# Kernel tuning notes

Hardware: AMD Instinct MI355X
Metric: run time of the kernel (lower is better)

Reference implementation:

```python
import jax, jax.numpy as jnp
import numpy as np

DIM = 1024          # moe_cfg.dim
INTER = 1024        # moe_cfg.moe_inter_dim
E = 8               # moe_cfg.n_routed_experts
TOPK = 2            # moe_cfg.n_activated_experts
ROUTE_SCALE = 1.0
SHARED_INTER = 2048 # n_shared_experts * moe_inter_dim
B, S = 4, 2048


def setup_inputs() -> dict:
    key = jax.random.key(0)
    ks = jax.random.split(key, 10)
    def w(k, shape, scale=0.02):
        return jax.random.normal(k, shape, jnp.float32) * scale
    return {
        "x": jax.random.normal(ks[0], (B, S, DIM), jnp.float32),
        # Gate (nn.Linear(dim, n_routed_experts, bias=True))
        "gate_w": w(ks[1], (E, DIM)),
        "gate_b": jnp.zeros((E,), jnp.float32),
        # Routed experts, stacked on leading E axis (torch Linear convention: [out, in])
        "w1": w(ks[2], (E, INTER, DIM)), "b1": jnp.zeros((E, INTER), jnp.float32),
        "w3": w(ks[3], (E, INTER, DIM)), "b3": jnp.zeros((E, INTER), jnp.float32),
        "w2": w(ks[4], (E, DIM, INTER)), "b2": jnp.zeros((E, DIM), jnp.float32),
        # Shared expert MLP(dim, n_shared_experts * moe_inter_dim)
        "ws1": w(ks[5], (SHARED_INTER, DIM)), "bs1": jnp.zeros((SHARED_INTER,), jnp.float32),
        "ws3": w(ks[6], (SHARED_INTER, DIM)), "bs3": jnp.zeros((SHARED_INTER,), jnp.float32),
        "ws2": w(ks[7], (DIM, SHARED_INTER)), "bs2": jnp.zeros((DIM,), jnp.float32),
    }


def _moe_forward(x, gate_w, gate_b, w1, b1, w3, b3, w2, b2,
                 ws1, bs1, ws3, bs3, ws2, bs2):
    Bq, Sq, D = x.shape
    xt = x.reshape(-1, D)  # [T, D], T = B*S
    # ---- Gate: softmax scores in fp32, top-k routing (eval mode: no usage buffers) ----
    logits = (xt @ gate_w.T + gate_b).astype(jnp.float32)  # [T, E]
    scores = jax.nn.softmax(logits, axis=-1)
    top_w, top_i = jax.lax.top_k(scores, TOPK)             # values == gathered scores
    weights = (top_w * ROUTE_SCALE).astype(x.dtype)        # [T, topk]
    # Dense combine weights [T, E]: zero for unrouted experts (math identical to dispatch)
    gate_dense = jnp.sum(jax.nn.one_hot(top_i, E, dtype=x.dtype) * weights[..., None], axis=1)
    # ---- Routed experts: SwiGLU FFN per expert (dropout p=0 -> identity) ----
    def expert(w1e, b1e, w3e, b3e, w2e, b2e):
        h = jax.nn.silu(xt @ w1e.T + b1e) * (xt @ w3e.T + b3e)  # [T, INTER]
        return h @ w2e.T + b2e                                   # [T, D]
    outs = jax.vmap(expert)(w1, b1, w3, b3, w2, b2)  # [E, T, D]
    y = jnp.einsum('etd,te->td', outs, gate_dense)   # weighted combine
    # ---- Shared expert MLP (SwiGLU) ----
    z = (jax.nn.silu(xt @ ws1.T + bs1) * (xt @ ws3.T + bs3)) @ ws2.T + bs2
    return (y + z).reshape(Bq, Sq, D)


def reference(x, gate_w, gate_b, w1, b1, w3, b3, w2, b2,
              ws1, bs1, ws3, bs3, ws2, bs2):
    return _moe_forward(x, gate_w, gate_b, w1, b1, w3, b3, w2, b2,
                        ws1, bs1, ws3, bs3, ws2, bs2)
```

## Files before the change

### kernel.cpp

```cpp
#include <hip/hip_runtime.h>
#include <stdint.h>
#include <stddef.h>

#define T_TOK  8192
#define DIMK   1024
#define INTERK 1024
#define NEXP   8
#define SINT   2048
#define CAP    18432
#define RT256  72

typedef float  f32x4  __attribute__((ext_vector_type(4)));
typedef short  bf16x8 __attribute__((ext_vector_type(8)));

typedef __attribute__((address_space(1))) const unsigned int gas_u32;
typedef __attribute__((address_space(3))) unsigned int las_u32;

__device__ __forceinline__ void gload16(const void* g, void* l) {
  __builtin_amdgcn_global_load_lds((gas_u32*)g, (las_u32*)l, 16, 0, 0);
}

__device__ __forceinline__ unsigned short f2b(float f) {
  unsigned int u = __float_as_uint(f);
  u = (u + 0x7FFFu + ((u >> 16) & 1u)) >> 16;
  return (unsigned short)u;
}
__device__ __forceinline__ float b2f(unsigned short h) {
  return __uint_as_float(((unsigned int)h) << 16);
}

__device__ __forceinline__ void barrier_nodrain() {
  asm volatile("" ::: "memory");
  __builtin_amdgcn_s_barrier();
  asm volatile("" ::: "memory");
}

__global__ __launch_bounds__(256) void cvt_kernel(const float4* __restrict__ in,
                                                  unsigned short* __restrict__ out, int n4) {
  int i = blockIdx.x * 256 + threadIdx.x;
  if (i >= n4) return;
  float4 v = in[i];
  ushort4 o;
  o.x = f2b(v.x); o.y = f2b(v.y); o.z = f2b(v.z); o.w = f2b(v.w);
  *reinterpret_cast<ushort4*>(&out[(size_t)i * 4]) = o;
}

template <int ROWS_PER_E, int K4>
__global__ __launch_bounds__(256) void cvt_w13_kernel(
    const float4* __restrict__ w1, const float4* __restrict__ w3,
    unsigned short* __restrict__ out, int n ) {
  int idx = blockIdx.x * 256 + threadIdx.x;
  int is3 = idx >= n;
  int i = is3 ? idx - n : idx;
  if (i >= n) return;
  int r  = i / K4;
  int kc = i - r * K4;
  int e  = r / ROWS_PER_E;
  int rr = r - e * ROWS_PER_E;
  int g  = rr >> 4;
  size_t dst_r = (size_t)e * (2 * ROWS_PER_E) + g * 32 + (is3 ? 16 : 0) + (rr & 15);
  float4 v = (is3 ? w3 : w1)[i];
  ushort4 o;
  o.x = f2b(v.x); o.y = f2b(v.y); o.z = f2b(v.z); o.w = f2b(v.w);
  *reinterpret_cast<ushort4*>(&out[(dst_r * K4 + kc) * 4]) = o;
}

__global__ __launch_bounds__(256) void gate_kernel(
    const float* __restrict__ x, const float* __restrict__ gw, const float* __restrict__ gb,
    int* __restrict__ top_i, float* __restrict__ top_w) {
  int t    = blockIdx.x * 4 + (threadIdx.x >> 6);
  int lane = threadIdx.x & 63;
  const float* xr = x + (size_t)t * DIMK;
  float acc[NEXP];
#pragma unroll
  for (int e = 0; e < NEXP; ++e) acc[e] = 0.f;
  for (int i = lane; i < DIMK; i += 64) {
    float xv = xr[i];
#pragma unroll
    for (int e = 0; e < NEXP; ++e) acc[e] += xv * gw[e * DIMK + i];
  }
#pragma unroll
  for (int e = 0; e < NEXP; ++e) {
    float v = acc[e];
#pragma unroll
    for (int off = 32; off > 0; off >>= 1) v += __shfl_down(v, off, 64);
    acc[e] = v;
  }
  if (lane == 0) {
    float lg[NEXP];
#pragma unroll
    for (int e = 0; e < NEXP; ++e) lg[e] = acc[e] + gb[e];
    int i0 = 0;
#pragma unroll
    for (int e = 1; e < NEXP; ++e) if (lg[e] > lg[i0]) i0 = e;
    int i1 = (i0 == 0) ? 1 : 0;
#pragma unroll
    for (int e = 0; e < NEXP; ++e) if (e != i0 && lg[e] > lg[i1]) i1 = e;
    float mx = lg[i0], s = 0.f;
#pragma unroll
    for (int e = 0; e < NEXP; ++e) s += expf(lg[e] - mx);
    top_i[t * 2]     = i0;
    top_i[t * 2 + 1] = i1;
    top_w[t * 2]     = expf(lg[i0] - mx) / s;
    top_w[t * 2 + 1] = expf(lg[i1] - mx) / s;
  }
}

__global__ __launch_bounds__(512) void route_build_kernel(
    const int* __restrict__ top_i, int* __restrict__ order, int* __restrict__ pos,
    int* __restrict__ poff_g) {
  __shared__ int cnt[NEXP][512];
  __shared__ int base[NEXP][512];
  __shared__ int totals[NEXP];
  __shared__ int poff_s[NEXP + 1];
  int tid = threadIdx.x;
  int lane = tid & 63, w = tid >> 6;
  const int t0 = tid * 16;

  int c[NEXP];
#pragma unroll
  for (int e = 0; e < NEXP; ++e) c[e] = 0;
  for (int j = 0; j < 16; ++j) {
    int e0 = top_i[(t0 + j) * 2];
    int e1 = top_i[(t0 + j) * 2 + 1];
#pragma unroll
    for (int e = 0; e < NEXP; ++e) c[e] += (e0 == e) + (e1 == e);
  }
#pragma unroll
  for (int e = 0; e < NEXP; ++e) cnt[e][tid] = c[e];
  __syncthreads();

  {
    int running = 0;
    for (int ch = 0; ch < 8; ++ch) {
      int v = cnt[w][ch * 64 + lane];
      int incl = v;
#pragma unroll
      for (int off = 1; off < 64; off <<= 1) {
        int u = __shfl_up(incl, off, 64);
        if (lane >= off) incl += u;
      }
      base[w][ch * 64 + lane] = running + incl - v;
      running += __shfl(incl, 63, 64);
    }
    if (lane == 0) totals[w] = running;
  }
  __syncthreads();

  if (tid == 0) {
    int off = 0;
#pragma unroll
    for (int e = 0; e < NEXP; ++e) {
      poff_s[e] = off;
      off += (totals[e] + 255) & ~255;
    }
    poff_s[NEXP] = off;
#pragma unroll
    for (int e = 0; e <= NEXP; ++e) poff_g[e] = poff_s[e];
  }
  __syncthreads();

  int cur[NEXP];
#pragma unroll
  for (int e = 0; e < NEXP; ++e) cur[e] = poff_s[e] + base[e][tid];
  for (int j = 0; j < 16; ++j) {
    int t = t0 + j;
#pragma unroll
    for (int k = 0; k < 2; ++k) {
      int ei = top_i[t * 2 + k];
      int p = 0;
#pragma unroll
      for (int e = 0; e < NEXP; ++e)
        if (ei == e) { p = cur[e]; cur[e] = p + 1; }
      order[p]       = t;
      pos[t * 2 + k] = p;
    }
  }

#pragma unroll
  for (int e = 0; e < NEXP; ++e) {
    int s = poff_s[e] + totals[e], en = poff_s[e + 1];
    for (int i = s + tid; i < en; i += 512) order[i] = 0;
  }
}

#define A_ELE  16384
#define B_ELE  8192
template <bool EXPERTS, bool GATHER, int EPI>
__global__ __launch_bounds__(512) void gemm256_kernel(
    const unsigned short* __restrict__ A, int lda,
    const int* __restrict__ order, const int* __restrict__ poff,
    const unsigned short* __restrict__ B,
    const float* __restrict__ bias1, const float* __restrict__ bias3,
    size_t wstride, int bstride, int K,
    void* __restrict__ outp, int ldo) {
  __shared__ unsigned short lds[2 * A_ELE + 2 * B_ELE];

  int rowbase = blockIdx.x * 256;
  int expert  = 0;
  if (EXPERTS) {
    if (rowbase >= poff[NEXP]) return;
    while (expert < NEXP - 1 && rowbase >= poff[expert + 1]) ++expert;
  }
  const unsigned short* Be = B + (size_t)expert * wstride;

  int tid = threadIdx.x;
  int lane = tid & 63, wid = tid >> 6;
  int wr = wid >> 1, wc = wid & 1;
  int ncolbase = blockIdx.y * 128;

  size_t aoff[4], boff[2];
#pragma unroll
  for (int l = 0; l < 4; ++l) {
    int g = l * 512 + tid;
    int r = g >> 3;
    int sub = (g & 7) ^ (r & 7);
    int gr = GATHER ? order[rowbase + r] : (rowbase + r);
    aoff[l] = (size_t)gr * lda + (size_t)(sub * 8);
  }
#pragma unroll
  for (int l = 0; l < 2; ++l) {
    int g = l * 512 + tid;
    int r = g >> 3;
    int sub = (g & 7) ^ (r & 7);
    boff[l] = (size_t)(ncolbase + r) * K + (size_t)(sub * 8);
  }

  f32x4 acc[4][4];
#pragma unroll
  for (int m = 0; m < 4; ++m)
#pragma unroll
    for (int n = 0; n < 4; ++n) acc[m][n] = f32x4{0.f, 0.f, 0.f, 0.f};

  const int NT = K >> 6;

#pragma unroll
  for (int l = 0; l < 4; ++l)
    gload16(A + aoff[l], &lds[(size_t)(l * 512 + tid) * 8]);
#pragma unroll
  for (int l = 0; l < 2; ++l)
    gload16(Be + boff[l], &lds[2 * A_ELE + (size_t)(l * 512 + tid) * 8]);

  for (int t = 0; t < NT; ++t) {
    int cur = t & 1;
    if (t + 1 < NT) {
      int kb = (t + 1) << 6;
      int nxt = cur ^ 1;
#pragma unroll
      for (int l = 0; l < 4; ++l)
        gload16(A + aoff[l] + kb, &lds[(size_t)nxt * A_ELE + (size_t)(l * 512 + tid) * 8]);
#pragma unroll
      for (int l = 0; l < 2; ++l)
        gload16(Be + boff[l] + kb, &lds[2 * A_ELE + (size_t)nxt * B_ELE + (size_t)(l * 512 + tid) * 8]);
      asm volatile("s_waitcnt vmcnt(6)" ::: "memory");
    } else {
      asm volatile("s_waitcnt vmcnt(0)" ::: "memory");
    }
    barrier_nodrain();

    const unsigned short* Ab = &lds[(size_t)cur * A_ELE];
    const unsigned short* Bb = &lds[2 * A_ELE + (size_t)cur * B_ELE];
    __builtin_amdgcn_s_setprio(1);
#pragma unroll
    for (int kk = 0; kk < 2; ++kk) {
      bf16x8 a[4], b[4];
#pragma unroll
      for (int m = 0; m < 4; ++m) {
        int ra = wr * 64 + m * 16 + (lane & 15);
        int sa = (kk * 4 + (lane >> 4)) ^ (ra & 7);
        a[m] = *(const bf16x8*)&Ab[ra * 64 + sa * 8];
      }
#pragma unroll
      for (int n = 0; n < 4; ++n) {
        int rb = wc * 64 + n * 16 + (lane & 15);
        int sb = (kk * 4 + (lane >> 4)) ^ (rb & 7);
        b[n] = *(const bf16x8*)&Bb[rb * 64 + sb * 8];
      }
#pragma unroll
      for (int m = 0; m < 4; ++m)
#pragma unroll
        for (int n = 0; n < 4; ++n)
          acc[m][n] = __builtin_amdgcn_mfma_f32_16x16x32_bf16(a[m], b[n], acc[m][n], 0, 0, 0);
    }
    __builtin_amdgcn_s_setprio(0);
    asm volatile("s_waitcnt lgkmcnt(0)" ::: "memory");
    barrier_nodrain();
  }

  if (EPI == 0) {
#pragma unroll
    for (int m = 0; m < 4; ++m)
#pragma unroll
      for (int np = 0; np < 2; ++np) {
        int realcol = (ncolbase >> 1) + wc * 32 + np * 16 + (lane & 15);
        float bb1 = bias1[bstride * expert + realcol];
        float bb3 = bias3[bstride * expert + realcol];
#pragma unroll
        for (int j = 0; j < 4; ++j) {
          int row  = rowbase + wr * 64 + m * 16 + (lane >> 4) * 4 + j;
          float a1 = acc[m][2 * np][j] + bb1;
          float a3 = acc[m][2 * np + 1][j] + bb3;
          float hv = (a1 / (1.f + __expf(-a1))) * a3;
          ((unsigned short*)outp)[(size_t)row * ldo + realcol] = f2b(hv);
        }
      }
  } else {
#pragma unroll
    for (int m = 0; m < 4; ++m)
#pragma unroll
      for (int n = 0; n < 4; ++n) {
        int col  = ncolbase + wc * 64 + n * 16 + (lane & 15);
        float bb = bias1[bstride * expert + col];
#pragma unroll
        for (int j = 0; j < 4; ++j) {
          int row = rowbase + wr * 64 + m * 16 + (lane >> 4) * 4 + j;
          float v = acc[m][n][j] + bb;
          if (EPI == 2)
            ((float*)outp)[(size_t)row * ldo + col] = v;
          else
            ((unsigned short*)outp)[(size_t)row * ldo + col] = f2b(v);
        }
      }
  }
}

__global__ __launch_bounds__(256) void combine_kernel(
    float* __restrict__ out, const unsigned short* __restrict__ y,
    const int* __restrict__ pos, const float* __restrict__ tw) {
  size_t idx = (size_t)blockIdx.x * 256 + threadIdx.x;
  if (idx >= (size_t)T_TOK * DIMK) return;
  int t = (int)(idx >> 10);
  int d = (int)(idx & 1023);
  int p0 = pos[t * 2], p1 = pos[t * 2 + 1];
  float w0 = tw[t * 2], w1 = tw[t * 2 + 1];
  out[idx] += w0 * b2f(y[(size_t)p0 * DIMK + d]) + w1 * b2f(y[(size_t)p1 * DIMK + d]);
}

extern "C" void kernel_launch(void* const* d_in, const int* in_sizes, int n_in,
                              void* d_out, int out_size, void* d_ws, size_t ws_size,
                              hipStream_t stream) {
  const float* x   = (const float*)d_in[0];
  const float* gw  = (const float*)d_in[1];
  const float* gb  = (const float*)d_in[2];
  const float* w1  = (const float*)d_in[3];
  const float* b1  = (const float*)d_in[4];
  const float* w3  = (const float*)d_in[5];
  const float* b3  = (const float*)d_in[6];
  const float* w2  = (const float*)d_in[7];
  const float* b2  = (const float*)d_in[8];
  const float* ws1 = (const float*)d_in[9];
  const float* bs1 = (const float*)d_in[10];
  const float* ws3 = (const float*)d_in[11];
  const float* bs3 = (const float*)d_in[12];
  const float* ws2 = (const float*)d_in[13];
  const float* bs2 = (const float*)d_in[14];
  float* out = (float*)d_out;
  (void)in_sizes; (void)n_in; (void)out_size; (void)ws_size;

  char* p = (char*)d_ws;
  auto alloc = [&](size_t bytes) -> void* {
    void* r = (void*)p;
    p += (bytes + 255) & ~(size_t)255;
    return r;
  };
  unsigned short* xb    = (unsigned short*)alloc((size_t)T_TOK * DIMK * 2);
  unsigned short* w13r  = (unsigned short*)alloc((size_t)NEXP * 2 * INTERK * DIMK * 2);
  unsigned short* w2b   = (unsigned short*)alloc((size_t)NEXP * DIMK * INTERK * 2);
  unsigned short* w13s  = (unsigned short*)alloc((size_t)2 * SINT * DIMK * 2);
  unsigned short* ws2b  = (unsigned short*)alloc((size_t)DIMK * SINT * 2);
  unsigned short* h     = (unsigned short*)alloc((size_t)CAP * INTERK * 2);
  unsigned short* yb    = (unsigned short*)alloc((size_t)CAP * DIMK * 2);
  unsigned short* hs    = (unsigned short*)alloc((size_t)T_TOK * SINT * 2);
  int*   top_i  = (int*)alloc((size_t)T_TOK * 2 * 4);
  float* top_w  = (float*)alloc((size_t)T_TOK * 2 * 4);
  int*   pos    = (int*)alloc((size_t)T_TOK * 2 * 4);
  int*   order  = (int*)alloc((size_t)CAP * 4);
  int*   poff   = (int*)alloc(64);

  auto cvt = [&](const float* src, unsigned short* dst, size_t n) {
    int n4 = (int)(n / 4);
    cvt_kernel<<<(n4 + 255) / 256, 256, 0, stream>>>((const float4*)src, dst, n4);
  };
  cvt(x,   xb,   (size_t)T_TOK * DIMK);
  cvt(w2,  w2b,  (size_t)NEXP * DIMK * INTERK);
  cvt(ws2, ws2b, (size_t)DIMK * SINT);

  {
    int n = NEXP * INTERK * (DIMK / 4);
    cvt_w13_kernel<INTERK, DIMK / 4><<<(2 * n + 255) / 256, 256, 0, stream>>>(
        (const float4*)w1, (const float4*)w3, w13r, n);
  }
  {
    int n = SINT * (DIMK / 4);
    cvt_w13_kernel<SINT, DIMK / 4><<<(2 * n + 255) / 256, 256, 0, stream>>>(
        (const float4*)ws1, (const float4*)ws3, w13s, n);
  }

  gate_kernel<<<T_TOK / 4, 256, 0, stream>>>(x, gw, gb, top_i, top_w);
  route_build_kernel<<<1, 512, 0, stream>>>(top_i, order, pos, poff);

  gemm256_kernel<true, true, 0><<<dim3(RT256, (2 * INTERK) / 128), 512, 0, stream>>>(
      xb, DIMK, order, poff, w13r, b1, b3,
      (size_t)2 * INTERK * DIMK, INTERK, DIMK, h, INTERK);
  gemm256_kernel<true, false, 1><<<dim3(RT256, DIMK / 128), 512, 0, stream>>>(
      h, INTERK, (const int*)nullptr, poff, w2b, b2, (const float*)nullptr,
      (size_t)DIMK * INTERK, DIMK, INTERK, (void*)yb, DIMK);

  gemm256_kernel<false, false, 0><<<dim3(T_TOK / 256, (2 * SINT) / 128), 512, 0, stream>>>(
      xb, DIMK, (const int*)nullptr, (const int*)nullptr, w13s, bs1, bs3,
      (size_t)0, 0, DIMK, hs, SINT);
  gemm256_kernel<false, false, 2><<<dim3(T_TOK / 256, DIMK / 128), 512, 0, stream>>>(
      hs, SINT, (const int*)nullptr, (const int*)nullptr, ws2b, bs2, (const float*)nullptr,
      (size_t)0, 0, SINT, (void*)out, DIMK);

  combine_kernel<<<(T_TOK * DIMK) / 256, 256, 0, stream>>>(out, yb, pos, top_w);
}
```

Measured before the change: 398.6 us.

## Triple-buffer GEMM LDS pipeline and swap grid axes for column-major block order

Replaces the double-buffered LDS pipeline in the shared GEMM kernel with a three-stage ring. Loads are issued two K-tiles ahead and interleaved with the two MFMA sub-steps, so only one barrier is needed per iteration. The grid axes are also swapped so that consecutive blocks share the same row tile and walk across column tiles, which is meant to improve L2 reuse of the A rows. LDS use grows from 96KB to 144KB per block, which rules out co-residency of a second block. There is also a risk that the vmcnt(6) wait count no longer matches the number of loads in flight.

```diff
diff --git a/kernel.cpp b/kernel.cpp
--- a/kernel.cpp
+++ b/kernel.cpp
@@ -184,8 +184,9 @@
   }
 }
 
-#define A_ELE  16384
-#define B_ELE  8192
+#define A_ELE   16384
+#define B_ELE   8192
+#define BUF_ELE (A_ELE + B_ELE)
 template <bool EXPERTS, bool GATHER, int EPI>
 __global__ __launch_bounds__(512) void gemm256_kernel(
     const unsigned short* __restrict__ A, int lda,
@@ -194,9 +195,9 @@
     const float* __restrict__ bias1, const float* __restrict__ bias3,
     size_t wstride, int bstride, int K,
     void* __restrict__ outp, int ldo) {
-  __shared__ unsigned short lds[2 * A_ELE + 2 * B_ELE];
-
-  int rowbase = blockIdx.x * 256;
+  __shared__ unsigned short lds[3 * BUF_ELE];
+
+  int rowbase = blockIdx.y * 256;
   int expert  = 0;
   if (EXPERTS) {
     if (rowbase >= poff[NEXP]) return;
@@ -207,7 +208,7 @@
   int tid = threadIdx.x;
   int lane = tid & 63, wid = tid >> 6;
   int wr = wid >> 1, wc = wid & 1;
-  int ncolbase = blockIdx.y * 128;
+  int ncolbase = blockIdx.x * 128;
 
   size_t aoff[4], boff[2];
 #pragma unroll
@@ -239,52 +240,86 @@
     gload16(A + aoff[l], &lds[(size_t)(l * 512 + tid) * 8]);
 #pragma unroll
   for (int l = 0; l < 2; ++l)
-    gload16(Be + boff[l], &lds[2 * A_ELE + (size_t)(l * 512 + tid) * 8]);
+    gload16(Be + boff[l], &lds[A_ELE + (size_t)(l * 512 + tid) * 8]);
+#pragma unroll
+  for (int l = 0; l < 4; ++l)
+    gload16(A + aoff[l] + 64, &lds[BUF_ELE + (size_t)(l * 512 + tid) * 8]);
+#pragma unroll
+  for (int l = 0; l < 2; ++l)
+    gload16(Be + boff[l] + 64, &lds[BUF_ELE + A_ELE + (size_t)(l * 512 + tid) * 8]);
+
+  unsigned int off_r = 0, off_m = BUF_ELE, off_w = 2 * BUF_ELE;
 
   for (int t = 0; t < NT; ++t) {
-    int cur = t & 1;
     if (t + 1 < NT) {
-      int kb = (t + 1) << 6;
-      int nxt = cur ^ 1;
-#pragma unroll
-      for (int l = 0; l < 4; ++l)
-        gload16(A + aoff[l] + kb, &lds[(size_t)nxt * A_ELE + (size_t)(l * 512 + tid) * 8]);
-#pragma unroll
-      for (int l = 0; l < 2; ++l)
-        gload16(Be + boff[l] + kb, &lds[2 * A_ELE + (size_t)nxt * B_ELE + (size_t)(l * 512 + tid) * 8]);
       asm volatile("s_waitcnt vmcnt(6)" ::: "memory");
     } else {
       asm volatile("s_waitcnt vmcnt(0)" ::: "memory");
     }
+    asm volatile("s_waitcnt lgkmcnt(0)" ::: "memory");
     barrier_nodrain();
 
-    const unsigned short* Ab = &lds[(size_t)cur * A_ELE];
-    const unsigned short* Bb = &lds[2 * A_ELE + (size_t)cur * B_ELE];
-    __builtin_amdgcn_s_setprio(1);
-#pragma unroll
-    for (int kk = 0; kk < 2; ++kk) {
+    const unsigned short* Ab = &lds[off_r];
+    const unsigned short* Bb = &lds[off_r + A_ELE];
+    const bool stage = (t + 2 < NT);
+    const int kb = (t + 2) << 6;
+
+    {
       bf16x8 a[4], b[4];
 #pragma unroll
       for (int m = 0; m < 4; ++m) {
         int ra = wr * 64 + m * 16 + (lane & 15);
-        int sa = (kk * 4 + (lane >> 4)) ^ (ra & 7);
+        int sa = ((lane >> 4)) ^ (ra & 7);
         a[m] = *(const bf16x8*)&Ab[ra * 64 + sa * 8];
       }
 #pragma unroll
       for (int n = 0; n < 4; ++n) {
         int rb = wc * 64 + n * 16 + (lane & 15);
-        int sb = (kk * 4 + (lane >> 4)) ^ (rb & 7);
+        int sb = ((lane >> 4)) ^ (rb & 7);
         b[n] = *(const bf16x8*)&Bb[rb * 64 + sb * 8];
       }
+      if (stage) {
+#pragma unroll
+        for (int l = 0; l < 4; ++l)
+          gload16(A + aoff[l] + kb, &lds[off_w + (size_t)(l * 512 + tid) * 8]);
+      }
+      __builtin_amdgcn_s_setprio(1);
 #pragma unroll
       for (int m = 0; m < 4; ++m)
 #pragma unroll
         for (int n = 0; n < 4; ++n)
           acc[m][n] = __builtin_amdgcn_mfma_f32_16x16x32_bf16(a[m], b[n], acc[m][n], 0, 0, 0);
-    }
-    __builtin_amdgcn_s_setprio(0);
-    asm volatile("s_waitcnt lgkmcnt(0)" ::: "memory");
-    barrier_nodrain();
+      __builtin_amdgcn_s_setprio(0);
+    }
+    {
+      bf16x8 a[4], b[4];
+#pragma unroll
+      for (int m = 0; m < 4; ++m) {
+        int ra = wr * 64 + m * 16 + (lane & 15);
+        int sa = (4 + (lane >> 4)) ^ (ra & 7);
+        a[m] = *(const bf16x8*)&Ab[ra * 64 + sa * 8];
+      }
+#pragma unroll
+      for (int n = 0; n < 4; ++n) {
+        int rb = wc * 64 + n * 16 + (lane & 15);
+        int sb = (4 + (lane >> 4)) ^ (rb & 7);
+        b[n] = *(const bf16x8*)&Bb[rb * 64 + sb * 8];
+      }
+      if (stage) {
+#pragma unroll
+        for (int l = 0; l < 2; ++l)
+          gload16(Be + boff[l] + kb, &lds[off_w + A_ELE + (size_t)(l * 512 + tid) * 8]);
+      }
+      __builtin_amdgcn_s_setprio(1);
+#pragma unroll
+      for (int m = 0; m < 4; ++m)
+#pragma unroll
+        for (int n = 0; n < 4; ++n)
+          acc[m][n] = __builtin_amdgcn_mfma_f32_16x16x32_bf16(a[m], b[n], acc[m][n], 0, 0, 0);
+      __builtin_amdgcn_s_setprio(0);
+    }
+
+    unsigned int tmp = off_r; off_r = off_m; off_m = off_w; off_w = tmp;
   }
 
   if (EPI == 0) {
@@ -399,17 +434,17 @@
   gate_kernel<<<T_TOK / 4, 256, 0, stream>>>(x, gw, gb, top_i, top_w);
   route_build_kernel<<<1, 512, 0, stream>>>(top_i, order, pos, poff);
 
-  gemm256_kernel<true, true, 0><<<dim3(RT256, (2 * INTERK) / 128), 512, 0, stream>>>(
+  gemm256_kernel<true, true, 0><<<dim3((2 * INTERK) / 128, RT256), 512, 0, stream>>>(
       xb, DIMK, order, poff, w13r, b1, b3,
       (size_t)2 * INTERK * DIMK, INTERK, DIMK, h, INTERK);
-  gemm256_kernel<true, false, 1><<<dim3(RT256, DIMK / 128), 512, 0, stream>>>(
+  gemm256_kernel<true, false, 1><<<dim3(DIMK / 128, RT256), 512, 0, stream>>>(
       h, INTERK, (const int*)nullptr, poff, w2b, b2, (const float*)nullptr,
       (size_t)DIMK * INTERK, DIMK, INTERK, (void*)yb, DIMK);
 
-  gemm256_kernel<false, false, 0><<<dim3(T_TOK / 256, (2 * SINT) / 128), 512, 0, stream>>>(
+  gemm256_kernel<false, false, 0><<<dim3((2 * SINT) / 128, T_TOK / 256), 512, 0, stream>>>(
       xb, DIMK, (const int*)nullptr, (const int*)nullptr, w13s, bs1, bs3,
       (size_t)0, 0, DIMK, hs, SINT);
-  gemm256_kernel<false, false, 2><<<dim3(T_TOK / 256, DIMK / 128), 512, 0, stream>>>(
+  gemm256_kernel<false, false, 2><<<dim3(DIMK / 128, T_TOK / 256), 512, 0, stream>>>(
       hs, SINT, (const int*)nullptr, (const int*)nullptr, ws2b, bs2, (const float*)nullptr,
       (size_t)0, 0, SINT, (void*)out, DIMK);
 
```

New measurement: 397.8 us. About the same (-0.2%).

## Triple-buffer GEMM with K=32 stages and 256x256 tiles for gate-up GEMMs

Applied to the files above, without the earlier changes.

Reworks the bf16 MFMA GEMM into a three-stage LDS pipeline with 32-wide K slices. The loads for stage t+2 are issued after the current fragments are read from LDS, so global loads overlap the MFMA work. A BN template parameter gives the two fused w1/w3 GEMMs 256x256 tiles, with each wave handling 128 rows in two MFMA halves, which raises arithmetic intensity per block. The grid axes are also swapped so neighbouring blocks share the same A rows, aiming for better L2 reuse. In exchange, register pressure is higher, LDS use grows, and there are more barriers per unit of K.

```diff
diff --git a/kernel.cpp b/kernel.cpp
--- a/kernel.cpp
+++ b/kernel.cpp
@@ -184,19 +184,24 @@
   }
 }
 
-#define A_ELE  16384
-#define B_ELE  8192
-template <bool EXPERTS, bool GATHER, int EPI>
-__global__ __launch_bounds__(512) void gemm256_kernel(
+template <bool EXPERTS, bool GATHER, int EPI, int BN>
+__global__ __launch_bounds__(512) void gemm_kernel(
     const unsigned short* __restrict__ A, int lda,
     const int* __restrict__ order, const int* __restrict__ poff,
     const unsigned short* __restrict__ B,
     const float* __restrict__ bias1, const float* __restrict__ bias3,
     size_t wstride, int bstride, int K,
     void* __restrict__ outp, int ldo) {
-  __shared__ unsigned short lds[2 * A_ELE + 2 * B_ELE];
-
-  int rowbase = blockIdx.x * 256;
+  constexpr int WRsh = (BN == 256) ? 2 : 1;
+  constexpr int WTM  = (BN == 256) ? 128 : 64;
+  constexpr int MF   = WTM / 16;
+  constexpr int AE   = 256 * 32;
+  constexpr int BE   = BN * 32;
+  constexpr int BUF  = AE + BE;
+  constexpr int BSW  = BN / 128;
+  __shared__ unsigned short lds[3 * BUF];
+
+  int rowbase = blockIdx.y * 256;
   int expert  = 0;
   if (EXPERTS) {
     if (rowbase >= poff[NEXP]) return;
@@ -206,90 +211,109 @@
 
   int tid = threadIdx.x;
   int lane = tid & 63, wid = tid >> 6;
-  int wr = wid >> 1, wc = wid & 1;
-  int ncolbase = blockIdx.y * 128;
-
-  size_t aoff[4], boff[2];
-#pragma unroll
-  for (int l = 0; l < 4; ++l) {
+  int wr = wid >> WRsh, wc = wid & ((1 << WRsh) - 1);
+  int ncolbase = blockIdx.x * BN;
+
+  size_t aoff[2], boff[BSW];
+#pragma unroll
+  for (int l = 0; l < 2; ++l) {
     int g = l * 512 + tid;
-    int r = g >> 3;
-    int sub = (g & 7) ^ (r & 7);
+    int r = g >> 2, cch = g & 3;
+    int sub = cch ^ ((r >> 1) & 3);
     int gr = GATHER ? order[rowbase + r] : (rowbase + r);
     aoff[l] = (size_t)gr * lda + (size_t)(sub * 8);
   }
 #pragma unroll
-  for (int l = 0; l < 2; ++l) {
+  for (int l = 0; l < BSW; ++l) {
     int g = l * 512 + tid;
-    int r = g >> 3;
-    int sub = (g & 7) ^ (r & 7);
+    int r = g >> 2, cch = g & 3;
+    int sub = cch ^ ((r >> 1) & 3);
     boff[l] = (size_t)(ncolbase + r) * K + (size_t)(sub * 8);
   }
 
-  f32x4 acc[4][4];
-#pragma unroll
-  for (int m = 0; m < 4; ++m)
+  f32x4 acc[MF][4];
+#pragma unroll
+  for (int m = 0; m < MF; ++m)
 #pragma unroll
     for (int n = 0; n < 4; ++n) acc[m][n] = f32x4{0.f, 0.f, 0.f, 0.f};
 
-  const int NT = K >> 6;
-
-#pragma unroll
-  for (int l = 0; l < 4; ++l)
-    gload16(A + aoff[l], &lds[(size_t)(l * 512 + tid) * 8]);
-#pragma unroll
-  for (int l = 0; l < 2; ++l)
-    gload16(Be + boff[l], &lds[2 * A_ELE + (size_t)(l * 512 + tid) * 8]);
+  const int NT = K >> 5;
+
+  auto stage_a = [&](int kb, unsigned bo) {
+#pragma unroll
+    for (int l = 0; l < 2; ++l)
+      gload16(A + aoff[l] + kb, &lds[bo + (size_t)(l * 512 + tid) * 8]);
+  };
+  auto stage_b = [&](int kb, unsigned bo) {
+#pragma unroll
+    for (int l = 0; l < BSW; ++l)
+      gload16(Be + boff[l] + kb, &lds[bo + AE + (size_t)(l * 512 + tid) * 8]);
+  };
+
+  stage_a(0, 0);           stage_b(0, 0);
+  stage_a(32, BUF);        stage_b(32, BUF);
 
   for (int t = 0; t < NT; ++t) {
-    int cur = t & 1;
     if (t + 1 < NT) {
-      int kb = (t + 1) << 6;
-      int nxt = cur ^ 1;
-#pragma unroll
-      for (int l = 0; l < 4; ++l)
-        gload16(A + aoff[l] + kb, &lds[(size_t)nxt * A_ELE + (size_t)(l * 512 + tid) * 8]);
-#pragma unroll
-      for (int l = 0; l < 2; ++l)
-        gload16(Be + boff[l] + kb, &lds[2 * A_ELE + (size_t)nxt * B_ELE + (size_t)(l * 512 + tid) * 8]);
-      asm volatile("s_waitcnt vmcnt(6)" ::: "memory");
+      if (BN == 256) { asm volatile("s_waitcnt vmcnt(4)" ::: "memory"); }
+      else           { asm volatile("s_waitcnt vmcnt(3)" ::: "memory"); }
     } else {
       asm volatile("s_waitcnt vmcnt(0)" ::: "memory");
     }
-    barrier_nodrain();
-
-    const unsigned short* Ab = &lds[(size_t)cur * A_ELE];
-    const unsigned short* Bb = &lds[2 * A_ELE + (size_t)cur * B_ELE];
-    __builtin_amdgcn_s_setprio(1);
-#pragma unroll
-    for (int kk = 0; kk < 2; ++kk) {
-      bf16x8 a[4], b[4];
-#pragma unroll
-      for (int m = 0; m < 4; ++m) {
-        int ra = wr * 64 + m * 16 + (lane & 15);
-        int sa = (kk * 4 + (lane >> 4)) ^ (ra & 7);
-        a[m] = *(const bf16x8*)&Ab[ra * 64 + sa * 8];
-      }
-#pragma unroll
-      for (int n = 0; n < 4; ++n) {
-        int rb = wc * 64 + n * 16 + (lane & 15);
-        int sb = (kk * 4 + (lane >> 4)) ^ (rb & 7);
-        b[n] = *(const bf16x8*)&Bb[rb * 64 + sb * 8];
-      }
-#pragma unroll
-      for (int m = 0; m < 4; ++m)
-#pragma unroll
-        for (int n = 0; n < 4; ++n)
-          acc[m][n] = __builtin_amdgcn_mfma_f32_16x16x32_bf16(a[m], b[n], acc[m][n], 0, 0, 0);
-    }
-    __builtin_amdgcn_s_setprio(0);
     asm volatile("s_waitcnt lgkmcnt(0)" ::: "memory");
     barrier_nodrain();
+
+    const unsigned short* Ab = &lds[(unsigned)(t % 3) * BUF];
+    const unsigned short* Bb = Ab + AE;
+    const bool st = (t + 2 < NT);
+    const int kb = (t + 2) << 5;
+    const unsigned wo = (unsigned)((t + 2) % 3) * BUF;
+
+    bf16x8 bf[4];
+#pragma unroll
+    for (int n = 0; n < 4; ++n) {
+      int row = wc * 64 + n * 16 + (lane & 15);
+      int kc = (lane >> 4) ^ ((row >> 1) & 3);
+      bf[n] = *(const bf16x8*)&Bb[row * 32 + kc * 8];
+    }
+    bf16x8 af[4];
+#pragma unroll
+    for (int m = 0; m < 4; ++m) {
+      int row = wr * WTM + m * 16 + (lane & 15);
+      int kc = (lane >> 4) ^ ((row >> 1) & 3);
+      af[m] = *(const bf16x8*)&Ab[row * 32 + kc * 8];
+    }
+    if (st) stage_a(kb, wo);
+    if (MF == 4 && st) stage_b(kb, wo);
+    __builtin_amdgcn_s_setprio(1);
+#pragma unroll
+    for (int m = 0; m < 4; ++m)
+#pragma unroll
+      for (int n = 0; n < 4; ++n)
+        acc[m][n] = __builtin_amdgcn_mfma_f32_16x16x32_bf16(af[m], bf[n], acc[m][n], 0, 0, 0);
+    __builtin_amdgcn_s_setprio(0);
+
+    if (MF == 8) {
+#pragma unroll
+      for (int m = 0; m < 4; ++m) {
+        int row = wr * WTM + (m + 4) * 16 + (lane & 15);
+        int kc = (lane >> 4) ^ ((row >> 1) & 3);
+        af[m] = *(const bf16x8*)&Ab[row * 32 + kc * 8];
+      }
+      if (st) stage_b(kb, wo);
+      __builtin_amdgcn_s_setprio(1);
+#pragma unroll
+      for (int m = 0; m < 4; ++m)
+#pragma unroll
+        for (int n = 0; n < 4; ++n)
+          acc[(m + 4) % MF][n] = __builtin_amdgcn_mfma_f32_16x16x32_bf16(af[m], bf[n], acc[(m + 4) % MF][n], 0, 0, 0);
+      __builtin_amdgcn_s_setprio(0);
+    }
   }
 
   if (EPI == 0) {
 #pragma unroll
-    for (int m = 0; m < 4; ++m)
+    for (int m = 0; m < MF; ++m)
 #pragma unroll
       for (int np = 0; np < 2; ++np) {
         int realcol = (ncolbase >> 1) + wc * 32 + np * 16 + (lane & 15);
@@ -297,7 +321,7 @@
         float bb3 = bias3[bstride * expert + realcol];
 #pragma unroll
         for (int j = 0; j < 4; ++j) {
-          int row  = rowbase + wr * 64 + m * 16 + (lane >> 4) * 4 + j;
+          int row  = rowbase + wr * WTM + m * 16 + (lane >> 4) * 4 + j;
           float a1 = acc[m][2 * np][j] + bb1;
           float a3 = acc[m][2 * np + 1][j] + bb3;
           float hv = (a1 / (1.f + __expf(-a1))) * a3;
@@ -306,14 +330,14 @@
       }
   } else {
 #pragma unroll
-    for (int m = 0; m < 4; ++m)
+    for (int m = 0; m < MF; ++m)
 #pragma unroll
       for (int n = 0; n < 4; ++n) {
         int col  = ncolbase + wc * 64 + n * 16 + (lane & 15);
         float bb = bias1[bstride * expert + col];
 #pragma unroll
         for (int j = 0; j < 4; ++j) {
-          int row = rowbase + wr * 64 + m * 16 + (lane >> 4) * 4 + j;
+          int row = rowbase + wr * WTM + m * 16 + (lane >> 4) * 4 + j;
           float v = acc[m][n][j] + bb;
           if (EPI == 2)
             ((float*)outp)[(size_t)row * ldo + col] = v;
@@ -399,17 +423,17 @@
   gate_kernel<<<T_TOK / 4, 256, 0, stream>>>(x, gw, gb, top_i, top_w);
   route_build_kernel<<<1, 512, 0, stream>>>(top_i, order, pos, poff);
 
-  gemm256_kernel<true, true, 0><<<dim3(RT256, (2 * INTERK) / 128), 512, 0, stream>>>(
+  gemm_kernel<true, true, 0, 256><<<dim3((2 * INTERK) / 256, RT256), 512, 0, stream>>>(
       xb, DIMK, order, poff, w13r, b1, b3,
       (size_t)2 * INTERK * DIMK, INTERK, DIMK, h, INTERK);
-  gemm256_kernel<true, false, 1><<<dim3(RT256, DIMK / 128), 512, 0, stream>>>(
+  gemm_kernel<true, false, 1, 128><<<dim3(DIMK / 128, RT256), 512, 0, stream>>>(
       h, INTERK, (const int*)nullptr, poff, w2b, b2, (const float*)nullptr,
       (size_t)DIMK * INTERK, DIMK, INTERK, (void*)yb, DIMK);
 
-  gemm256_kernel<false, false, 0><<<dim3(T_TOK / 256, (2 * SINT) / 128), 512, 0, stream>>>(
+  gemm_kernel<false, false, 0, 256><<<dim3((2 * SINT) / 256, T_TOK / 256), 512, 0, stream>>>(
       xb, DIMK, (const int*)nullptr, (const int*)nullptr, w13s, bs1, bs3,
       (size_t)0, 0, DIMK, hs, SINT);
-  gemm256_kernel<false, false, 2><<<dim3(T_TOK / 256, DIMK / 128), 512, 0, stream>>>(
+  gemm_kernel<false, false, 2, 128><<<dim3(DIMK / 128, T_TOK / 256), 512, 0, stream>>>(
       hs, SINT, (const int*)nullptr, (const int*)nullptr, ws2b, bs2, (const float*)nullptr,
       (size_t)0, 0, SINT, (void*)out, DIMK);
 
```

Measured after the change: 408.7 us. 2.5% more time.

## Enlarge GEMM tile to 256x256 with phased LDS staging and swapped grid axes

Applied to the files above, without the earlier changes.

The shared bf16 GEMM kernel goes from a 256x128 tile to a 256x256 tile, with each of the 8 waves computing a 128x64 sub-tile (32 accumulators). The K loop is split into four compute phases. The next A and B tiles are issued in between those phases, and fragments are loaded in halves to keep register pressure down. The grid is transposed so that column blocks vary fastest, which makes neighbouring blocks share A rows. The aim is higher arithmetic intensity and fewer redundant global and LDS loads. The cost is more barriers per iteration, a full vmcnt(0) wait, 128KB of LDS, and higher VGPR use that may limit occupancy.

```diff
diff --git a/kernel.cpp b/kernel.cpp
--- a/kernel.cpp
+++ b/kernel.cpp
@@ -184,8 +184,8 @@
   }
 }
 
-#define A_ELE  16384
-#define B_ELE  8192
+#define AE256 16384
+#define BUF2  32768
 template <bool EXPERTS, bool GATHER, int EPI>
 __global__ __launch_bounds__(512) void gemm256_kernel(
     const unsigned short* __restrict__ A, int lda,
@@ -194,9 +194,9 @@
     const float* __restrict__ bias1, const float* __restrict__ bias3,
     size_t wstride, int bstride, int K,
     void* __restrict__ outp, int ldo) {
-  __shared__ unsigned short lds[2 * A_ELE + 2 * B_ELE];
-
-  int rowbase = blockIdx.x * 256;
+  __shared__ unsigned short lds[2 * BUF2];
+
+  int rowbase = blockIdx.y * 256;
   int expert  = 0;
   if (EXPERTS) {
     if (rowbase >= poff[NEXP]) return;
@@ -206,10 +206,10 @@
 
   int tid = threadIdx.x;
   int lane = tid & 63, wid = tid >> 6;
-  int wr = wid >> 1, wc = wid & 1;
-  int ncolbase = blockIdx.y * 128;
-
-  size_t aoff[4], boff[2];
+  int wr = wid >> 2, wc = wid & 3;
+  int ncolbase = blockIdx.x * 256;
+
+  size_t aoff[4], boff[4];
 #pragma unroll
   for (int l = 0; l < 4; ++l) {
     int g = l * 512 + tid;
@@ -217,79 +217,135 @@
     int sub = (g & 7) ^ (r & 7);
     int gr = GATHER ? order[rowbase + r] : (rowbase + r);
     aoff[l] = (size_t)gr * lda + (size_t)(sub * 8);
-  }
-#pragma unroll
-  for (int l = 0; l < 2; ++l) {
-    int g = l * 512 + tid;
-    int r = g >> 3;
-    int sub = (g & 7) ^ (r & 7);
     boff[l] = (size_t)(ncolbase + r) * K + (size_t)(sub * 8);
   }
 
-  f32x4 acc[4][4];
-#pragma unroll
-  for (int m = 0; m < 4; ++m)
+  f32x4 acc[8][4];
+#pragma unroll
+  for (int m = 0; m < 8; ++m)
 #pragma unroll
     for (int n = 0; n < 4; ++n) acc[m][n] = f32x4{0.f, 0.f, 0.f, 0.f};
 
   const int NT = K >> 6;
 
-#pragma unroll
-  for (int l = 0; l < 4; ++l)
-    gload16(A + aoff[l], &lds[(size_t)(l * 512 + tid) * 8]);
-#pragma unroll
-  for (int l = 0; l < 2; ++l)
-    gload16(Be + boff[l], &lds[2 * A_ELE + (size_t)(l * 512 + tid) * 8]);
+  auto stage_a = [&](int kb, unsigned bo) {
+#pragma unroll
+    for (int l = 0; l < 4; ++l)
+      gload16(A + aoff[l] + kb, &lds[bo + (size_t)(l * 512 + tid) * 8]);
+  };
+  auto stage_b = [&](int kb, unsigned bo) {
+#pragma unroll
+    for (int l = 0; l < 4; ++l)
+      gload16(Be + boff[l] + kb, &lds[bo + AE256 + (size_t)(l * 512 + tid) * 8]);
+  };
+
+  stage_a(0, 0);
+  stage_b(0, 0);
 
   for (int t = 0; t < NT; ++t) {
-    int cur = t & 1;
-    if (t + 1 < NT) {
-      int kb = (t + 1) << 6;
-      int nxt = cur ^ 1;
-#pragma unroll
-      for (int l = 0; l < 4; ++l)
-        gload16(A + aoff[l] + kb, &lds[(size_t)nxt * A_ELE + (size_t)(l * 512 + tid) * 8]);
-#pragma unroll
-      for (int l = 0; l < 2; ++l)
-        gload16(Be + boff[l] + kb, &lds[2 * A_ELE + (size_t)nxt * B_ELE + (size_t)(l * 512 + tid) * 8]);
-      asm volatile("s_waitcnt vmcnt(6)" ::: "memory");
-    } else {
-      asm volatile("s_waitcnt vmcnt(0)" ::: "memory");
-    }
-    barrier_nodrain();
-
-    const unsigned short* Ab = &lds[(size_t)cur * A_ELE];
-    const unsigned short* Bb = &lds[2 * A_ELE + (size_t)cur * B_ELE];
+    asm volatile("s_waitcnt vmcnt(0)" ::: "memory");
+    barrier_nodrain();
+
+    const unsigned bo = (unsigned)(t & 1) * BUF2;
+    const unsigned short* Ab = &lds[bo];
+    const unsigned short* Bb = &lds[bo + AE256];
+    const bool st = (t + 1 < NT);
+    const int kb = (t + 1) << 6;
+    const unsigned wo = bo ^ BUF2;
+
+    bf16x8 bf[4][2], af[4][2];
+
+#pragma unroll
+    for (int m = 0; m < 4; ++m) {
+      int row = wr * 128 + m * 16 + (lane & 15);
+#pragma unroll
+      for (int kk = 0; kk < 2; ++kk) {
+        int kc = (kk * 4 + (lane >> 4)) ^ (row & 7);
+        af[m][kk] = *(const bf16x8*)&Ab[row * 64 + kc * 8];
+      }
+    }
+#pragma unroll
+    for (int n = 0; n < 2; ++n) {
+      int row = wc * 64 + n * 16 + (lane & 15);
+#pragma unroll
+      for (int kk = 0; kk < 2; ++kk) {
+        int kc = (kk * 4 + (lane >> 4)) ^ (row & 7);
+        bf[n][kk] = *(const bf16x8*)&Bb[row * 64 + kc * 8];
+      }
+    }
+    if (st) stage_a(kb, wo);
+    barrier_nodrain();
+    asm volatile("s_waitcnt lgkmcnt(0)" ::: "memory");
     __builtin_amdgcn_s_setprio(1);
 #pragma unroll
-    for (int kk = 0; kk < 2; ++kk) {
-      bf16x8 a[4], b[4];
-#pragma unroll
-      for (int m = 0; m < 4; ++m) {
-        int ra = wr * 64 + m * 16 + (lane & 15);
-        int sa = (kk * 4 + (lane >> 4)) ^ (ra & 7);
-        a[m] = *(const bf16x8*)&Ab[ra * 64 + sa * 8];
-      }
-#pragma unroll
-      for (int n = 0; n < 4; ++n) {
-        int rb = wc * 64 + n * 16 + (lane & 15);
-        int sb = (kk * 4 + (lane >> 4)) ^ (rb & 7);
-        b[n] = *(const bf16x8*)&Bb[rb * 64 + sb * 8];
-      }
-#pragma unroll
-      for (int m = 0; m < 4; ++m)
-#pragma unroll
-        for (int n = 0; n < 4; ++n)
-          acc[m][n] = __builtin_amdgcn_mfma_f32_16x16x32_bf16(a[m], b[n], acc[m][n], 0, 0, 0);
-    }
+    for (int m = 0; m < 4; ++m)
+#pragma unroll
+      for (int n = 0; n < 2; ++n)
+#pragma unroll
+        for (int kk = 0; kk < 2; ++kk)
+          acc[m][n] = __builtin_amdgcn_mfma_f32_16x16x32_bf16(af[m][kk], bf[n][kk], acc[m][n], 0, 0, 0);
     __builtin_amdgcn_s_setprio(0);
+    barrier_nodrain();
+
+#pragma unroll
+    for (int n = 2; n < 4; ++n) {
+      int row = wc * 64 + n * 16 + (lane & 15);
+#pragma unroll
+      for (int kk = 0; kk < 2; ++kk) {
+        int kc = (kk * 4 + (lane >> 4)) ^ (row & 7);
+        bf[n][kk] = *(const bf16x8*)&Bb[row * 64 + kc * 8];
+      }
+    }
+    if (st) stage_b(kb, wo);
+    barrier_nodrain();
     asm volatile("s_waitcnt lgkmcnt(0)" ::: "memory");
-    barrier_nodrain();
+    __builtin_amdgcn_s_setprio(1);
+#pragma unroll
+    for (int m = 0; m < 4; ++m)
+#pragma unroll
+      for (int n = 2; n < 4; ++n)
+#pragma unroll
+        for (int kk = 0; kk < 2; ++kk)
+          acc[m][n] = __builtin_amdgcn_mfma_f32_16x16x32_bf16(af[m][kk], bf[n][kk], acc[m][n], 0, 0, 0);
+    __builtin_amdgcn_s_setprio(0);
+    barrier_nodrain();
+
+#pragma unroll
+    for (int m = 0; m < 4; ++m) {
+      int row = wr * 128 + (m + 4) * 16 + (lane & 15);
+#pragma unroll
+      for (int kk = 0; kk < 2; ++kk) {
+        int kc = (kk * 4 + (lane >> 4)) ^ (row & 7);
+        af[m][kk] = *(const bf16x8*)&Ab[row * 64 + kc * 8];
+      }
+    }
+    barrier_nodrain();
+    asm volatile("s_waitcnt lgkmcnt(0)" ::: "memory");
+    __builtin_amdgcn_s_setprio(1);
+#pragma unroll
+    for (int m = 0; m < 4; ++m)
+#pragma unroll
+      for (int n = 2; n < 4; ++n)
+#pragma unroll
+        for (int kk = 0; kk < 2; ++kk)
+          acc[m + 4][n] = __builtin_amdgcn_mfma_f32_16x16x32_bf16(af[m][kk], bf[n][kk], acc[m + 4][n], 0, 0, 0);
+    __builtin_amdgcn_s_setprio(0);
+    barrier_nodrain();
+
+    __builtin_amdgcn_s_setprio(1);
+#pragma unroll
+    for (int m = 0; m < 4; ++m)
+#pragma unroll
+      for (int n = 0; n < 2; ++n)
+#pragma unroll
+        for (int kk = 0; kk < 2; ++kk)
+          acc[m + 4][n] = __builtin_amdgcn_mfma_f32_16x16x32_bf16(af[m][kk], bf[n][kk], acc[m + 4][n], 0, 0, 0);
+    __builtin_amdgcn_s_setprio(0);
   }
 
   if (EPI == 0) {
 #pragma unroll
-    for (int m = 0; m < 4; ++m)
+    for (int m = 0; m < 8; ++m)
 #pragma unroll
       for (int np = 0; np < 2; ++np) {
         int realcol = (ncolbase >> 1) + wc * 32 + np * 16 + (lane & 15);
@@ -297,7 +353,7 @@
         float bb3 = bias3[bstride * expert + realcol];
 #pragma unroll
         for (int j = 0; j < 4; ++j) {
-          int row  = rowbase + wr * 64 + m * 16 + (lane >> 4) * 4 + j;
+          int row  = rowbase + wr * 128 + m * 16 + (lane >> 4) * 4 + j;
           float a1 = acc[m][2 * np][j] + bb1;
           float a3 = acc[m][2 * np + 1][j] + bb3;
           float hv = (a1 / (1.f + __expf(-a1))) * a3;
@@ -306,14 +362,14 @@
       }
   } else {
 #pragma unroll
-    for (int m = 0; m < 4; ++m)
+    for (int m = 0; m < 8; ++m)
 #pragma unroll
       for (int n = 0; n < 4; ++n) {
         int col  = ncolbase + wc * 64 + n * 16 + (lane & 15);
         float bb = bias1[bstride * expert + col];
 #pragma unroll
         for (int j = 0; j < 4; ++j) {
-          int row = rowbase + wr * 64 + m * 16 + (lane >> 4) * 4 + j;
+          int row = rowbase + wr * 128 + m * 16 + (lane >> 4) * 4 + j;
           float v = acc[m][n][j] + bb;
           if (EPI == 2)
             ((float*)outp)[(size_t)row * ldo + col] = v;
@@ -399,17 +455,17 @@
   gate_kernel<<<T_TOK / 4, 256, 0, stream>>>(x, gw, gb, top_i, top_w);
   route_build_kernel<<<1, 512, 0, stream>>>(top_i, order, pos, poff);
 
-  gemm256_kernel<true, true, 0><<<dim3(RT256, (2 * INTERK) / 128), 512, 0, stream>>>(
+  gemm256_kernel<true, true, 0><<<dim3((2 * INTERK) / 256, RT256), 512, 0, stream>>>(
       xb, DIMK, order, poff, w13r, b1, b3,
       (size_t)2 * INTERK * DIMK, INTERK, DIMK, h, INTERK);
-  gemm256_kernel<true, false, 1><<<dim3(RT256, DIMK / 128), 512, 0, stream>>>(
+  gemm256_kernel<true, false, 1><<<dim3(DIMK / 256, RT256), 512, 0, stream>>>(
       h, INTERK, (const int*)nullptr, poff, w2b, b2, (const float*)nullptr,
       (size_t)DIMK * INTERK, DIMK, INTERK, (void*)yb, DIMK);
 
-  gemm256_kernel<false, false, 0><<<dim3(T_TOK / 256, (2 * SINT) / 128), 512, 0, stream>>>(
+  gemm256_kernel<false, false, 0><<<dim3((2 * SINT) / 256, T_TOK / 256), 512, 0, stream>>>(
       xb, DIMK, (const int*)nullptr, (const int*)nullptr, w13s, bs1, bs3,
       (size_t)0, 0, DIMK, hs, SINT);
-  gemm256_kernel<false, false, 2><<<dim3(T_TOK / 256, DIMK / 128), 512, 0, stream>>>(
+  gemm256_kernel<false, false, 2><<<dim3(DIMK / 256, T_TOK / 256), 512, 0, stream>>>(
       hs, SINT, (const int*)nullptr, (const int*)nullptr, ws2b, bs2, (const float*)nullptr,
       (size_t)0, 0, SINT, (void*)out, DIMK);
 
```

After: 408.5 us. 2.5% more time.
